# Optimization experiments

Measured on AMD Instinct MI355X. Metric: run time of the kernel, lower is better.

## Reference

```python
import jax, jax.numpy as jnp
import numpy as np

B, L, D, H = 2, 2048, 1024, 16
DH = D // H
TAU = 0.1


def setup_inputs() -> dict:
    key = jax.random.key(0)
    ks = jax.random.split(key, 12)
    s = 0.02
    return {
        "q_x": jax.random.normal(ks[0], (B, L, D), jnp.float32),
        "k_x": jax.random.normal(ks[1], (B, L, D), jnp.float32),
        "v_x": jax.random.normal(ks[2], (B, L, D), jnp.float32),
        "ec": jax.random.normal(ks[3], (B, L, D), jnp.float32),
        "Wq": jax.random.normal(ks[4], (D, D), jnp.float32) * s,
        "bq": jnp.zeros((D,), jnp.float32),
        "Wk": jax.random.normal(ks[5], (D, D), jnp.float32) * s,
        "bk": jnp.zeros((D,), jnp.float32),
        "Wv": jax.random.normal(ks[6], (D, D), jnp.float32) * s,
        "bv": jnp.zeros((D,), jnp.float32),
        "Wo": jax.random.normal(ks[7], (D, D), jnp.float32) * s,
        "bo": jnp.zeros((D,), jnp.float32),
    }


def reference(q_x, k_x, v_x, ec, Wq, bq, Wk, bk, Wv, bv, Wo, bo):
    # torch nn.Linear: y = x @ W.T + b
    Q = (q_x @ Wq.T + bq).reshape(B, L, H, DH).transpose(0, 2, 1, 3)   # [B,H,L,Dh]
    K = (k_x @ Wk.T + bk).reshape(B, -1, H, DH).transpose(0, 2, 1, 3)  # [B,H,S,Dh]
    V = (v_x @ Wv.T + bv).reshape(B, -1, H, DH).transpose(0, 2, 1, 3)  # [B,H,S,Dh]
    scores = jnp.einsum("bhld,bhsd->bhls", Q, K) / jnp.sqrt(jnp.float32(DH))
    w = jnp.nan_to_num(jax.nn.softmax(scores, axis=-1), nan=0.0)       # [B,H,L,S]
    # frequency gate per key position: sigmoid((mean|ec| - tau) * 10)
    gate = jax.nn.sigmoid((jnp.abs(ec).mean(-1) - TAU) * 10.0)          # [B,S]
    w = w * gate[:, None, None, :]
    out = jnp.einsum("bhls,bhsd->bhld", w, V)                           # [B,H,L,Dh]
    out = out.transpose(0, 2, 1, 3).reshape(B, L, D)
    return out @ Wo.T + bo
```

## Files before the change

### kernel.cpp

```cpp
#include <hip/hip_runtime.h>

typedef unsigned short u16;
typedef unsigned int u32;
typedef unsigned long long u64;
typedef __attribute__((ext_vector_type(8))) short bf16x8;
typedef __attribute__((ext_vector_type(4))) float f32x4;
typedef __attribute__((ext_vector_type(2))) unsigned int u32x2;
typedef __attribute__((ext_vector_type(4))) unsigned int u32x4;

#define B_ 2
#define L_ 2048
#define D_ 1024
#define H_ 16
#define M_ 4096

__device__ __forceinline__ u16 f2bf(float f) {
  u32 x = __builtin_bit_cast(u32, f);
  return (u16)((x + 0x7fffu + ((x >> 16) & 1u)) >> 16);
}
__device__ __forceinline__ u32 cvtpk(float lo, float hi) {
  u32 r;
  asm("v_cvt_pk_bf16_f32 %0, %1, %2" : "=v"(r) : "v"(lo), "v"(hi));
  return r;
}

__device__ __forceinline__ void lane_regroup(u32& a, u32& b) {
#if __has_builtin(__builtin_amdgcn_permlane32_swap) && \
    __has_builtin(__builtin_amdgcn_permlane16_swap)
  u32x2 r = __builtin_amdgcn_permlane32_swap(a, b, false, false);
  u32x2 t = __builtin_amdgcn_permlane16_swap(r.x, r.y, false, false);
  a = t.x;
  b = t.y;
#else
  asm("v_permlane32_swap_b32 %0, %1\n\t"
      "v_permlane16_swap_b32 %0, %1"
      : "+v"(a), "+v"(b));
#endif
}

__device__ __forceinline__ void gl2lds16(void* lds, const void* g) {
  __builtin_amdgcn_global_load_lds(
      (const __attribute__((address_space(1))) u32*)g,
      (__attribute__((address_space(3))) u32*)lds, 16, 0, 0);
}

__device__ __forceinline__ void wait_vm8() {
  asm volatile("s_waitcnt vmcnt(8)" ::: "memory");
}
__device__ __forceinline__ void wait_vm6() {
  asm volatile("s_waitcnt vmcnt(6)" ::: "memory");
}
__device__ __forceinline__ void wait_vm4() {
  asm volatile("s_waitcnt vmcnt(4)" ::: "memory");
}
__device__ __forceinline__ void wait_vm0() {
  asm volatile("s_waitcnt vmcnt(0)" ::: "memory");
}
__device__ __forceinline__ void bar() {
  asm volatile("" ::: "memory");
  __builtin_amdgcn_s_barrier();
  asm volatile("" ::: "memory");
}

__global__ void cvt_all(const float* __restrict__ q, const float* __restrict__ k,
                        const float* __restrict__ v, const float* __restrict__ wq,
                        const float* __restrict__ wk, const float* __restrict__ wv,
                        const float* __restrict__ wo, const float* __restrict__ ec,
                        u16* __restrict__ Xq, u16* __restrict__ Xk, u16* __restrict__ Xv,
                        u16* __restrict__ Wqb, u16* __restrict__ Wkb,
                        u16* __restrict__ Wvb, u16* __restrict__ Wob,
                        float* __restrict__ gate) {
  if (blockIdx.x >= 16384) {
    int row = (blockIdx.x - 16384) * 4 + (threadIdx.x >> 6);
    int lane = threadIdx.x & 63;
    const float4* p = (const float4*)(ec + (size_t)row * 1024);
    float s = 0.f;
#pragma unroll
    for (int i = 0; i < 4; i++) {
      float4 vv = p[i * 64 + lane];
      s += fabsf(vv.x) + fabsf(vv.y) + fabsf(vv.z) + fabsf(vv.w);
    }
#pragma unroll
    for (int m = 1; m < 64; m <<= 1) s += __shfl_xor(s, m);
    if (lane == 0) {
      float mean = s * (1.0f / 1024.0f);
      gate[row] = 1.0f / (1.0f + __expf(-(mean - 0.1f) * 10.0f));
    }
    return;
  }
  int i = blockIdx.x * 256 + threadIdx.x;
  const float* s;
  u16* d;
  int off;
  if (i < 3145728) {
    int t = i >> 20;
    off = i & 1048575;
    s = t == 0 ? q : t == 1 ? k : v;
    d = t == 0 ? Xq : t == 1 ? Xk : Xv;
  } else {
    int j = i - 3145728;
    int t = j >> 18;
    off = j & 262143;
    s = t == 0 ? wq : t == 1 ? wk : t == 2 ? wv : wo;
    d = t == 0 ? Wqb : t == 1 ? Wkb : t == 2 ? Wvb : Wob;
  }
  float4 vv = ((const float4*)s)[off];
  ((u64*)d)[off] = (u64)cvtpk(vv.x, vv.y) | ((u64)cvtpk(vv.z, vv.w) << 32);
}

__global__ __launch_bounds__(256, 2) void gemm_qkv(
    const u16* __restrict__ Xq, const u16* __restrict__ Xk, const u16* __restrict__ Xv,
    const u16* __restrict__ Wq, const u16* __restrict__ Wk, const u16* __restrict__ Wv,
    const float* __restrict__ bq, const float* __restrict__ bk,
    const float* __restrict__ bv, const float* __restrict__ gate,
    u16* __restrict__ Qo, u16* __restrict__ Ko, u16* __restrict__ Vt) {
  __shared__ char smem[65536];
  const int which = blockIdx.x >> 8;
  const u16* A = which == 0 ? Xq : which == 1 ? Xk : Xv;
  const u16* Bw = which == 0 ? Wq : which == 1 ? Wk : Wv;
  const float* bias = which == 0 ? bq : which == 1 ? bk : bv;
  const int bi = blockIdx.x & 255;
  const int tid = threadIdx.x;
  const int tm = bi >> 3;
  const int tn = bi & 7;
  const int w = tid >> 6, lane = tid & 63;
  const int c = lane & 15, g = lane >> 4;
  const int wr = (w >> 1) << 6, wc = (w & 1) << 6;
  const int srow = tid >> 3, sch = tid & 7;

  f32x4 acc[4][4] = {};

  auto stage = [&](int buf, int t) {
    char* As = smem + buf * 32768;
    char* Bs = As + 16384;
#pragma unroll
    for (int i = 0; i < 4; i++) {
      int row = i * 32 + srow;
      int chs = (sch ^ (row & 7)) << 3;
      gl2lds16(As + i * 4096 + w * 1024, A + (size_t)(tm * 128 + row) * 1024 + t * 64 + chs);
      gl2lds16(Bs + i * 4096 + w * 1024, Bw + (size_t)(tn * 128 + row) * 1024 + t * 64 + chs);
    }
  };

  stage(0, 0);
  for (int t = 0; t < 16; t++) {
    int cur = t & 1;
    if (t < 15) {
      stage(cur ^ 1, t + 1);
      wait_vm8();
    } else {
      wait_vm0();
    }
    bar();
    const char* As = smem + cur * 32768;
    const char* Bs = As + 16384;
#pragma unroll
    for (int kd = 0; kd < 2; kd++) {
      bf16x8 af[4], bfr[4];
#pragma unroll
      for (int fi = 0; fi < 4; fi++) {
        int ra = wr + fi * 16 + c;
        af[fi] = *(const bf16x8*)(As + ra * 128 + ((((kd << 2) | g) ^ (ra & 7)) << 4));
        int rb = wc + fi * 16 + c;
        bfr[fi] = *(const bf16x8*)(Bs + rb * 128 + ((((kd << 2) | g) ^ (rb & 7)) << 4));
      }
#pragma unroll
      for (int fi = 0; fi < 4; fi++)
#pragma unroll
        for (int fj = 0; fj < 4; fj++)
          acc[fi][fj] = __builtin_amdgcn_mfma_f32_16x16x32_bf16(af[fi], bfr[fj],
                                                                acc[fi][fj], 0, 0, 0);
    }
    bar();
  }

  if (which == 2) {
    u16* T = (u16*)smem;
    __syncthreads();
#pragma unroll
    for (int fi = 0; fi < 4; fi++) {
      int lr0 = wr + fi * 16 + g * 4;
      float4 gg = *(const float4*)(gate + tm * 128 + lr0);
#pragma unroll
      for (int fj = 0; fj < 4; fj++) {
        int lc = wc + fj * 16 + c;
        float bv2 = bias[tn * 128 + lc];
        T[lc * 136 + lr0 + 0] = f2bf((acc[fi][fj][0] + bv2) * gg.x);
        T[lc * 136 + lr0 + 1] = f2bf((acc[fi][fj][1] + bv2) * gg.y);
        T[lc * 136 + lr0 + 2] = f2bf((acc[fi][fj][2] + bv2) * gg.z);
        T[lc * 136 + lr0 + 3] = f2bf((acc[fi][fj][3] + bv2) * gg.w);
      }
    }
    __syncthreads();
    const int lc = tid >> 1, hf = tid & 1;
    const int vtrow = (tm >> 4) * 1024 + tn * 128 + lc;
    const int s0 = (tm & 15) * 128 + hf * 64;
    const char* Trow = (const char*)(T + lc * 136) + hf * 128;
    u16* dst = Vt + (size_t)vtrow * 2048 + s0;
#pragma unroll
    for (int j = 0; j < 8; j++)
      *(bf16x8*)(dst + j * 8) = *(const bf16x8*)(Trow + j * 16);
  } else {
    u16* Cout = which == 0 ? Qo : Ko;
    const float oscl = which == 0 ? 0.18033688011112042f : 1.0f;
    const int rowb = tm * 128 + wr + g * 4;
    const int colb = tn * 128 + wc + c;
#pragma unroll
    for (int fj = 0; fj < 4; fj++) {
      int col = colb + fj * 16;
      float bv2 = bias[col];
#pragma unroll
      for (int fi = 0; fi < 4; fi++) {
        int r0 = rowb + fi * 16;
#pragma unroll
        for (int r = 0; r < 4; r++)
          Cout[(size_t)(r0 + r) * 1024 + col] = f2bf((acc[fi][fj][r] + bv2) * oscl);
      }
    }
  }
}

__global__ __launch_bounds__(256, 2) void gemm_o(const u16* __restrict__ A,
                                                 const u16* __restrict__ Bw,
                                                 const float* __restrict__ bias,
                                                 float* __restrict__ Cout) {
  __shared__ char smem[49152];
  const int tid = threadIdx.x;
  const int tm = blockIdx.x >> 3;
  const int tn = blockIdx.x & 7;
  const int w = tid >> 6, lane = tid & 63;
  const int c = lane & 15, g = lane >> 4;
  const int wr = (w >> 1) << 5;
  const int wc = (w & 1) << 6;
  const int srow = tid >> 3, sch = tid & 7;

  f32x4 acc[2][4] = {};

  auto stage = [&](int buf, int t) {
    char* As = smem + buf * 24576;
    char* Bs = As + 8192;
#pragma unroll
    for (int i = 0; i < 2; i++) {
      int row = i * 32 + srow;
      int chs = (sch ^ (row & 7)) << 3;
      gl2lds16(As + i * 4096 + w * 1024, A + (size_t)(tm * 64 + row) * 1024 + t * 64 + chs);
    }
#pragma unroll
    for (int i = 0; i < 4; i++) {
      int row = i * 32 + srow;
      int chs = (sch ^ (row & 7)) << 3;
      gl2lds16(Bs + i * 4096 + w * 1024, Bw + (size_t)(tn * 128 + row) * 1024 + t * 64 + chs);
    }
  };

  stage(0, 0);
  for (int t = 0; t < 16; t++) {
    int cur = t & 1;
    if (t < 15) {
      stage(cur ^ 1, t + 1);
      wait_vm6();
    } else {
      wait_vm0();
    }
    bar();
    const char* As = smem + cur * 24576;
    const char* Bs = As + 8192;
#pragma unroll
    for (int kd = 0; kd < 2; kd++) {
      bf16x8 af[2], bfr[4];
#pragma unroll
      for (int fi = 0; fi < 2; fi++) {
        int ra = wr + fi * 16 + c;
        af[fi] = *(const bf16x8*)(As + ra * 128 + ((((kd << 2) | g) ^ (ra & 7)) << 4));
      }
#pragma unroll
      for (int fj = 0; fj < 4; fj++) {
        int rb = wc + fj * 16 + c;
        bfr[fj] = *(const bf16x8*)(Bs + rb * 128 + ((((kd << 2) | g) ^ (rb & 7)) << 4));
      }
#pragma unroll
      for (int fi = 0; fi < 2; fi++)
#pragma unroll
        for (int fj = 0; fj < 4; fj++)
          acc[fi][fj] = __builtin_amdgcn_mfma_f32_16x16x32_bf16(af[fi], bfr[fj],
                                                                acc[fi][fj], 0, 0, 0);
    }
    bar();
  }

  const int rowb = tm * 64 + wr + g * 4;
  const int colb = tn * 128 + wc + c;
#pragma unroll
  for (int fj = 0; fj < 4; fj++) {
    int col = colb + fj * 16;
    float bv2 = bias[col];
#pragma unroll
    for (int fi = 0; fi < 2; fi++) {
      int r0 = rowb + fi * 16;
#pragma unroll
      for (int r = 0; r < 4; r++)
        Cout[(size_t)(r0 + r) * 1024 + col] = acc[fi][fj][r] + bv2;
    }
  }
}

__global__ __launch_bounds__(256, 3) void attn_kernel(const u16* __restrict__ Qb,
                                                      const u16* __restrict__ Kb,
                                                      const u16* __restrict__ Vt,
                                                      u16* __restrict__ Ob) {
  __shared__ char asmem[49152];
  const int bi = blockIdx.x;
  const int bh = (bi & 7) | ((bi >> 7) << 3);
  const int qt = (bi >> 3) & 15;
  const int b = bh >> 4, h = bh & 15;
  const int tid = threadIdx.x, w = tid >> 6, lane = tid & 63;
  const int c = lane & 15, g = lane >> 4;
  const int qrow0 = b * L_ + qt * 128 + w * 32;

  bf16x8 qf[2][2];
#pragma unroll
  for (int fj = 0; fj < 2; fj++)
#pragma unroll
    for (int kd = 0; kd < 2; kd++)
      qf[fj][kd] = *(const bf16x8*)(Qb + (size_t)(qrow0 + fj * 16 + c) * D_ + h * 64 +
                                    kd * 32 + g * 8);

  const u32x4 onew = {0x3F803F80u, 0x3F803F80u, 0x3F803F80u, 0x3F803F80u};
  const bf16x8 one8 = __builtin_bit_cast(bf16x8, onew);

  f32x4 oacc[4][2] = {};
  f32x4 oaccD[2] = {};

  const int srow = tid >> 3, sch = tid & 7;
  const int vrow = tid >> 4, vch = tid & 15;

  auto stageK = [&](int buf, int kv) {
    char* KsB = asmem + buf * 16384;
    int sbase = kv * 128;
#pragma unroll
    for (int i = 0; i < 4; i++) {
      int kr = i * 32 + srow;
      gl2lds16(KsB + i * 4096 + w * 1024,
               Kb + (size_t)(b * L_ + sbase + kr) * D_ + h * 64 + ((sch ^ (kr & 7)) << 3));
    }
  };
  auto stageV = [&](int kv) {
    char* VsB = asmem + 32768;
    int sbase = kv * 128;
#pragma unroll
    for (int i = 0; i < 4; i++) {
      int vr = i * 16 + vrow;
      gl2lds16(VsB + i * 4096 + w * 1024,
               Vt + (size_t)(bh * 64 + vr) * 2048 + sbase + ((vch ^ (vr & 15)) << 3));
    }
  };

  stageK(0, 0);
  stageV(0);
  int buf = 0;
  for (int kv = 0; kv < 16; kv++) {
    if (kv < 15) {
      stageK(buf ^ 1, kv + 1);
      wait_vm8();
    } else {
      wait_vm4();
    }
    bar();
    const char* Ks = asmem + buf * 16384;
    const char* Vs = asmem + 32768;

    f32x4 st0[8] = {}, st1[8] = {};
    __builtin_amdgcn_s_setprio(1);
#pragma unroll
    for (int kd = 0; kd < 2; kd++) {
#pragma unroll
      for (int fi = 0; fi < 8; fi++) {
        int row = fi * 16 + c;
        bf16x8 kf = *(const bf16x8*)(Ks + row * 128 + ((((kd << 2) | g) ^ (c & 7)) << 4));
        st0[fi] = __builtin_amdgcn_mfma_f32_16x16x32_bf16(kf, qf[0][kd], st0[fi], 0, 0, 0);
        st1[fi] = __builtin_amdgcn_mfma_f32_16x16x32_bf16(kf, qf[1][kd], st1[fi], 0, 0, 0);
      }
    }
    __builtin_amdgcn_s_setprio(0);

    u32 pkA0[8], pkB0[8], pkA1[8], pkB1[8];
#pragma unroll
    for (int fi = 0; fi < 8; fi++) {
      pkA0[fi] = cvtpk(__builtin_amdgcn_exp2f(st0[fi][0]), __builtin_amdgcn_exp2f(st0[fi][1]));
      pkB0[fi] = cvtpk(__builtin_amdgcn_exp2f(st0[fi][2]), __builtin_amdgcn_exp2f(st0[fi][3]));
    }
#pragma unroll
    for (int fi = 0; fi < 8; fi++) {
      pkA1[fi] = cvtpk(__builtin_amdgcn_exp2f(st1[fi][0]), __builtin_amdgcn_exp2f(st1[fi][1]));
      pkB1[fi] = cvtpk(__builtin_amdgcn_exp2f(st1[fi][2]), __builtin_amdgcn_exp2f(st1[fi][3]));
    }

    if (kv < 15)
      wait_vm4();
    else
      wait_vm0();

    __builtin_amdgcn_s_setprio(1);
#pragma unroll
    for (int ks = 0; ks < 4; ks++) {
      u32 a0 = pkA0[2 * ks], b0 = pkA0[2 * ks + 1];
      lane_regroup(a0, b0);
      u32 a1 = pkB0[2 * ks], b1 = pkB0[2 * ks + 1];
      lane_regroup(a1, b1);
      u32x4 pw0 = {a0, a1, b0, b1};
      bf16x8 pf0 = __builtin_bit_cast(bf16x8, pw0);
      u32 e0 = pkA1[2 * ks], f0 = pkA1[2 * ks + 1];
      lane_regroup(e0, f0);
      u32 e1 = pkB1[2 * ks], f1 = pkB1[2 * ks + 1];
      lane_regroup(e1, f1);
      u32x4 pw1 = {e0, e1, f0, f1};
      bf16x8 pf1 = __builtin_bit_cast(bf16x8, pw1);
      oaccD[0] = __builtin_amdgcn_mfma_f32_16x16x32_bf16(one8, pf0, oaccD[0], 0, 0, 0);
      oaccD[1] = __builtin_amdgcn_mfma_f32_16x16x32_bf16(one8, pf1, oaccD[1], 0, 0, 0);
#pragma unroll
      for (int fd = 0; fd < 4; fd++) {
        int vr2 = fd * 16 + c;
        bf16x8 vf = *(const bf16x8*)(Vs + vr2 * 256 + ((((ks << 2) | g) ^ (vr2 & 15)) << 4));
        oacc[fd][0] = __builtin_amdgcn_mfma_f32_16x16x32_bf16(vf, pf0, oacc[fd][0], 0, 0, 0);
        oacc[fd][1] = __builtin_amdgcn_mfma_f32_16x16x32_bf16(vf, pf1, oacc[fd][1], 0, 0, 0);
      }
    }
    __builtin_amdgcn_s_setprio(0);
    bar();
    if (kv < 15) stageV(kv + 1);
    buf ^= 1;
  }

#pragma unroll
  for (int fj = 0; fj < 2; fj++) {
    float inv = 1.0f / oaccD[fj][0];
    size_t orow = (size_t)(qrow0 + fj * 16 + c) * D_ + h * 64;
#pragma unroll
    for (int fd = 0; fd < 4; fd++) {
      u64 pk = (u64)cvtpk(oacc[fd][fj][0] * inv, oacc[fd][fj][1] * inv) |
               ((u64)cvtpk(oacc[fd][fj][2] * inv, oacc[fd][fj][3] * inv) << 32);
      *(u64*)(Ob + orow + fd * 16 + g * 4) = pk;
    }
  }
}

extern "C" void kernel_launch(void* const* d_in, const int* in_sizes, int n_in,
                              void* d_out, int out_size, void* d_ws, size_t ws_size,
                              hipStream_t stream) {
  const float* q_x = (const float*)d_in[0];
  const float* k_x = (const float*)d_in[1];
  const float* v_x = (const float*)d_in[2];
  const float* ec = (const float*)d_in[3];
  const float* Wq = (const float*)d_in[4];
  const float* bq = (const float*)d_in[5];
  const float* Wk = (const float*)d_in[6];
  const float* bk = (const float*)d_in[7];
  const float* Wv = (const float*)d_in[8];
  const float* bv = (const float*)d_in[9];
  const float* Wo = (const float*)d_in[10];
  const float* bo = (const float*)d_in[11];

  char* ws = (char*)d_ws;
  const size_t MB = 1024 * 1024;
  u16* Wqb = (u16*)(ws + 0 * MB);
  u16* Wkb = (u16*)(ws + 2 * MB);
  u16* Wvb = (u16*)(ws + 4 * MB);
  u16* Wob = (u16*)(ws + 6 * MB);
  float* gatep = (float*)(ws + 8 * MB);
  u16* Xq = (u16*)(ws + 9 * MB);
  u16* Xk = (u16*)(ws + 17 * MB);
  u16* Xv = (u16*)(ws + 25 * MB);
  u16* Qb = (u16*)(ws + 33 * MB);
  u16* Kb = (u16*)(ws + 41 * MB);
  u16* Vtb = (u16*)(ws + 49 * MB);
  u16* Ab = Xk;

  cvt_all<<<17408, 256, 0, stream>>>(q_x, k_x, v_x, Wq, Wk, Wv, Wo, ec, Xq, Xk, Xv,
                                     Wqb, Wkb, Wvb, Wob, gatep);
  gemm_qkv<<<768, 256, 0, stream>>>(Xq, Xk, Xv, Wqb, Wkb, Wvb, bq, bk, bv, gatep, Qb,
                                    Kb, Vtb);
  attn_kernel<<<512, 256, 0, stream>>>(Qb, Kb, Vtb, Ab);
  gemm_o<<<512, 256, 0, stream>>>(Ab, Wob, bo, (float*)d_out);
}
```

Before: 115.4 us.

## Split attention block across eight waves with sixteen query rows each

The attention kernel now runs 512 threads per block: each wave handles 16 query rows instead of 32, with matching changes to the K/V staging loops and the vmcnt wait thresholds. Per-wave accumulators and score registers are halved, which lowers register pressure and raises the number of waves available to hide latency. In exchange, each K/V fragment read from LDS is reused by fewer MFMAs per wave, so LDS read traffic per FLOP roughly doubles, and barriers now synchronise eight waves instead of four.

```diff
diff --git a/kernel.cpp b/kernel.cpp
--- a/kernel.cpp
+++ b/kernel.cpp
@@ -52,6 +52,9 @@
 }
 __device__ __forceinline__ void wait_vm4() {
   asm volatile("s_waitcnt vmcnt(4)" ::: "memory");
+}
+__device__ __forceinline__ void wait_vm2() {
+  asm volatile("s_waitcnt vmcnt(2)" ::: "memory");
 }
 __device__ __forceinline__ void wait_vm0() {
   asm volatile("s_waitcnt vmcnt(0)" ::: "memory");
@@ -304,7 +307,7 @@
   }
 }
 
-__global__ __launch_bounds__(256, 3) void attn_kernel(const u16* __restrict__ Qb,
+__global__ __launch_bounds__(512, 4) void attn_kernel(const u16* __restrict__ Qb,
                                                       const u16* __restrict__ Kb,
                                                       const u16* __restrict__ Vt,
                                                       u16* __restrict__ Ob) {
@@ -315,43 +318,39 @@
   const int b = bh >> 4, h = bh & 15;
   const int tid = threadIdx.x, w = tid >> 6, lane = tid & 63;
   const int c = lane & 15, g = lane >> 4;
-  const int qrow0 = b * L_ + qt * 128 + w * 32;
-
-  bf16x8 qf[2][2];
-#pragma unroll
-  for (int fj = 0; fj < 2; fj++)
-#pragma unroll
-    for (int kd = 0; kd < 2; kd++)
-      qf[fj][kd] = *(const bf16x8*)(Qb + (size_t)(qrow0 + fj * 16 + c) * D_ + h * 64 +
-                                    kd * 32 + g * 8);
+  const int qrow0 = b * L_ + qt * 128 + w * 16;
+
+  bf16x8 qf[2];
+#pragma unroll
+  for (int kd = 0; kd < 2; kd++)
+    qf[kd] = *(const bf16x8*)(Qb + (size_t)(qrow0 + c) * D_ + h * 64 + kd * 32 + g * 8);
 
   const u32x4 onew = {0x3F803F80u, 0x3F803F80u, 0x3F803F80u, 0x3F803F80u};
   const bf16x8 one8 = __builtin_bit_cast(bf16x8, onew);
 
-  f32x4 oacc[4][2] = {};
-  f32x4 oaccD[2] = {};
-
-  const int srow = tid >> 3, sch = tid & 7;
-  const int vrow = tid >> 4, vch = tid & 15;
+  f32x4 oacc[4] = {};
+  f32x4 oaccD = {};
 
   auto stageK = [&](int buf, int kv) {
     char* KsB = asmem + buf * 16384;
     int sbase = kv * 128;
 #pragma unroll
-    for (int i = 0; i < 4; i++) {
-      int kr = i * 32 + srow;
-      gl2lds16(KsB + i * 4096 + w * 1024,
-               Kb + (size_t)(b * L_ + sbase + kr) * D_ + h * 64 + ((sch ^ (kr & 7)) << 3));
+    for (int i = 0; i < 2; i++) {
+      int kr = i * 64 + (tid >> 3);
+      gl2lds16(KsB + i * 8192 + w * 1024,
+               Kb + (size_t)(b * L_ + sbase + kr) * D_ + h * 64 +
+                   (((tid & 7) ^ (kr & 7)) << 3));
     }
   };
   auto stageV = [&](int kv) {
     char* VsB = asmem + 32768;
     int sbase = kv * 128;
 #pragma unroll
-    for (int i = 0; i < 4; i++) {
-      int vr = i * 16 + vrow;
-      gl2lds16(VsB + i * 4096 + w * 1024,
-               Vt + (size_t)(bh * 64 + vr) * 2048 + sbase + ((vch ^ (vr & 15)) << 3));
+    for (int i = 0; i < 2; i++) {
+      int vr = i * 32 + (tid >> 4);
+      gl2lds16(VsB + i * 8192 + w * 1024,
+               Vt + (size_t)(bh * 64 + vr) * 2048 + sbase +
+                   (((tid & 15) ^ (vr & 15)) << 3));
     }
   };
 
@@ -361,15 +360,15 @@
   for (int kv = 0; kv < 16; kv++) {
     if (kv < 15) {
       stageK(buf ^ 1, kv + 1);
-      wait_vm8();
+      wait_vm4();
     } else {
-      wait_vm4();
+      wait_vm2();
     }
     bar();
     const char* Ks = asmem + buf * 16384;
     const char* Vs = asmem + 32768;
 
-    f32x4 st0[8] = {}, st1[8] = {};
+    f32x4 st[8] = {};
     __builtin_amdgcn_s_setprio(1);
 #pragma unroll
     for (int kd = 0; kd < 2; kd++) {
@@ -377,52 +376,38 @@
       for (int fi = 0; fi < 8; fi++) {
         int row = fi * 16 + c;
         bf16x8 kf = *(const bf16x8*)(Ks + row * 128 + ((((kd << 2) | g) ^ (c & 7)) << 4));
-        st0[fi] = __builtin_amdgcn_mfma_f32_16x16x32_bf16(kf, qf[0][kd], st0[fi], 0, 0, 0);
-        st1[fi] = __builtin_amdgcn_mfma_f32_16x16x32_bf16(kf, qf[1][kd], st1[fi], 0, 0, 0);
+        st[fi] = __builtin_amdgcn_mfma_f32_16x16x32_bf16(kf, qf[kd], st[fi], 0, 0, 0);
       }
     }
     __builtin_amdgcn_s_setprio(0);
 
-    u32 pkA0[8], pkB0[8], pkA1[8], pkB1[8];
+    u32 pkA[8], pkB[8];
 #pragma unroll
     for (int fi = 0; fi < 8; fi++) {
-      pkA0[fi] = cvtpk(__builtin_amdgcn_exp2f(st0[fi][0]), __builtin_amdgcn_exp2f(st0[fi][1]));
-      pkB0[fi] = cvtpk(__builtin_amdgcn_exp2f(st0[fi][2]), __builtin_amdgcn_exp2f(st0[fi][3]));
-    }
-#pragma unroll
-    for (int fi = 0; fi < 8; fi++) {
-      pkA1[fi] = cvtpk(__builtin_amdgcn_exp2f(st1[fi][0]), __builtin_amdgcn_exp2f(st1[fi][1]));
-      pkB1[fi] = cvtpk(__builtin_amdgcn_exp2f(st1[fi][2]), __builtin_amdgcn_exp2f(st1[fi][3]));
+      pkA[fi] = cvtpk(__builtin_amdgcn_exp2f(st[fi][0]), __builtin_amdgcn_exp2f(st[fi][1]));
+      pkB[fi] = cvtpk(__builtin_amdgcn_exp2f(st[fi][2]), __builtin_amdgcn_exp2f(st[fi][3]));
     }
 
     if (kv < 15)
-      wait_vm4();
+      wait_vm2();
     else
       wait_vm0();
 
     __builtin_amdgcn_s_setprio(1);
 #pragma unroll
     for (int ks = 0; ks < 4; ks++) {
-      u32 a0 = pkA0[2 * ks], b0 = pkA0[2 * ks + 1];
+      u32 a0 = pkA[2 * ks], b0 = pkA[2 * ks + 1];
       lane_regroup(a0, b0);
-      u32 a1 = pkB0[2 * ks], b1 = pkB0[2 * ks + 1];
+      u32 a1 = pkB[2 * ks], b1 = pkB[2 * ks + 1];
       lane_regroup(a1, b1);
-      u32x4 pw0 = {a0, a1, b0, b1};
-      bf16x8 pf0 = __builtin_bit_cast(bf16x8, pw0);
-      u32 e0 = pkA1[2 * ks], f0 = pkA1[2 * ks + 1];
-      lane_regroup(e0, f0);
-      u32 e1 = pkB1[2 * ks], f1 = pkB1[2 * ks + 1];
-      lane_regroup(e1, f1);
-      u32x4 pw1 = {e0, e1, f0, f1};
-      bf16x8 pf1 = __builtin_bit_cast(bf16x8, pw1);
-      oaccD[0] = __builtin_amdgcn_mfma_f32_16x16x32_bf16(one8, pf0, oaccD[0], 0, 0, 0);
-      oaccD[1] = __builtin_amdgcn_mfma_f32_16x16x32_bf16(one8, pf1, oaccD[1], 0, 0, 0);
+      u32x4 pw = {a0, a1, b0, b1};
+      bf16x8 pf = __builtin_bit_cast(bf16x8, pw);
+      oaccD = __builtin_amdgcn_mfma_f32_16x16x32_bf16(one8, pf, oaccD, 0, 0, 0);
 #pragma unroll
       for (int fd = 0; fd < 4; fd++) {
         int vr2 = fd * 16 + c;
         bf16x8 vf = *(const bf16x8*)(Vs + vr2 * 256 + ((((ks << 2) | g) ^ (vr2 & 15)) << 4));
-        oacc[fd][0] = __builtin_amdgcn_mfma_f32_16x16x32_bf16(vf, pf0, oacc[fd][0], 0, 0, 0);
-        oacc[fd][1] = __builtin_amdgcn_mfma_f32_16x16x32_bf16(vf, pf1, oacc[fd][1], 0, 0, 0);
+        oacc[fd] = __builtin_amdgcn_mfma_f32_16x16x32_bf16(vf, pf, oacc[fd], 0, 0, 0);
       }
     }
     __builtin_amdgcn_s_setprio(0);
@@ -431,16 +416,13 @@
     buf ^= 1;
   }
 
-#pragma unroll
-  for (int fj = 0; fj < 2; fj++) {
-    float inv = 1.0f / oaccD[fj][0];
-    size_t orow = (size_t)(qrow0 + fj * 16 + c) * D_ + h * 64;
-#pragma unroll
-    for (int fd = 0; fd < 4; fd++) {
-      u64 pk = (u64)cvtpk(oacc[fd][fj][0] * inv, oacc[fd][fj][1] * inv) |
-               ((u64)cvtpk(oacc[fd][fj][2] * inv, oacc[fd][fj][3] * inv) << 32);
-      *(u64*)(Ob + orow + fd * 16 + g * 4) = pk;
-    }
+  float inv = 1.0f / oaccD[0];
+  size_t orow = (size_t)(qrow0 + c) * D_ + h * 64;
+#pragma unroll
+  for (int fd = 0; fd < 4; fd++) {
+    u64 pk = (u64)cvtpk(oacc[fd][0] * inv, oacc[fd][1] * inv) |
+             ((u64)cvtpk(oacc[fd][2] * inv, oacc[fd][3] * inv) << 32);
+    *(u64*)(Ob + orow + fd * 16 + g * 4) = pk;
   }
 }
 
@@ -479,6 +461,6 @@
                                      Wqb, Wkb, Wvb, Wob, gatep);
   gemm_qkv<<<768, 256, 0, stream>>>(Xq, Xk, Xv, Wqb, Wkb, Wvb, bq, bk, bv, gatep, Qb,
                                     Kb, Vtb);
-  attn_kernel<<<512, 256, 0, stream>>>(Qb, Kb, Vtb, Ab);
+  attn_kernel<<<512, 512, 0, stream>>>(Qb, Kb, Vtb, Ab);
   gemm_o<<<512, 256, 0, stream>>>(Ab, Wob, bo, (float*)d_out);
 }
```

Result: no change. 116.8 us (+1.2%).
